# Performance work log

Measured on AMD Instinct MI355X. Metric: run time of the kernel, lower is better.

Reference implementation:

```python
import math
import jax, jax.numpy as jnp
import numpy as np
from jax import lax

SAMPLE_RATE = 16000
BLOCK_SIZE = 64
B = 524288


def setup_inputs() -> dict:
    key = jax.random.key(0)
    k1, k2, k3 = jax.random.split(key, 3)
    fm_params = jax.random.uniform(k1, (B, 1, 6), dtype=jnp.float32)
    # realistic fundamentals in [50, 400) Hz; module clamps to >=1 anyway
    f0_hz = 50.0 + 350.0 * jax.random.uniform(k2, (B, 1), dtype=jnp.float32)
    phase_state = jax.random.uniform(k3, (B, 4), dtype=jnp.float32)
    return {"fm_params": fm_params, "f0_hz": f0_hz, "phase_state": phase_state}


def reference(fm_params, f0_hz, phase_state):
    # T == 1 (module requirement), so squeeze the frame dim everywhere.
    dtype = fm_params.dtype
    two_pi = 2.0 * math.pi

    f0 = jnp.clip(f0_hz[:, 0], 1.0, None)            # [B]
    p = fm_params[:, 0, :]                            # [B, 6]
    # parameter mappings (op1 mod depth p[:,0] is unused, as in the original)
    r1 = 0.25 + p[:, 1] * 15.75
    fb1 = p[:, 2] * 0.95
    d2 = p[:, 3] * 10.0
    r2 = 0.25 + p[:, 4] * 15.75
    fb2 = p[:, 5] * 0.95

    inc1 = two_pi * f0 * r1 / SAMPLE_RATE             # [B]
    inc2 = two_pi * f0 * r2 / SAMPLE_RATE

    start1 = phase_state[:, 0]                        # frame start phases
    start2 = phase_state[:, 1]
    last1_0 = phase_state[:, 2]                       # feedback buffers
    last2_0 = phase_state[:, 3]

    offsets = jnp.arange(BLOCK_SIZE, dtype=dtype)     # [S]
    # per-sample phases, scanned over the sample axis: [S, B]
    phase1 = start1[None, :] + offsets[:, None] * inc1[None, :]
    phase2 = start2[None, :] + offsets[:, None] * inc2[None, :]

    def step(carry, ph):
        l1, l2 = carry
        ph1, ph2 = ph
        o1 = jnp.sin(ph1 + fb1 * l1)                  # op1 with self-feedback
        o2 = jnp.sin(ph2 + d2 * o1 + fb2 * l2)        # op2 carrier, FM'd by op1
        return (o1, o2), o2

    (l1f, l2f), samples = lax.scan(step, (last1_0, last2_0), (phase1, phase2))
    audio = samples.T                                 # [B, S]

    rms = jnp.sqrt(jnp.mean(audio * audio, axis=-1, keepdims=True) + 1e-5)
    audio = audio / rms

    phase_end = jnp.stack(
        [
            (start1 + BLOCK_SIZE * inc1) % two_pi,
            (start2 + BLOCK_SIZE * inc2) % two_pi,
            l1f,
            l2f,
        ],
        axis=-1,
    )                                                 # [B, 4]
    return audio, phase_end
```

## Files before the change

### kernel.cpp

```cpp
#include <hip/hip_runtime.h>

#define NBLOCK 64

__device__ __forceinline__ float fast_sinf(float x) {
    float kf = rintf(x * 0.63661977236758134f);
    int   q  = (int)kf;
    float r = fmaf(kf, -1.5707963705062866f, x);
    r = fmaf(kf, 4.3711390001862171e-8f, r);
    float z = r * r;
    float s = fmaf(z, fmaf(z, -1.9515295891e-4f, 8.3321608736e-3f), -1.6666654611e-1f);
    float sinr = fmaf(z * r, s, r);
    float c = fmaf(z, fmaf(z, 2.4433157118e-5f, -1.3887316255e-3f), 4.1666645683e-2f);
    float cosr = fmaf(z, fmaf(z, c, -0.5f), 1.0f);
    float res = (q & 1) ? cosr : sinr;
    return (q & 2) ? -res : res;
}

__device__ __forceinline__ float mod_two_pi(float x) {
    const float Y = 6.2831853071795864769f;
    float kf = floorf(__fdiv_rn(x, Y));
    float m = fmaf(-kf, Y, x);
    if (m < 0.0f)  { kf -= 1.0f; m = fmaf(-kf, Y, x); }
    if (m >= Y)    { kf += 1.0f; m = fmaf(-kf, Y, x); }
    return m;
}

__global__ __launch_bounds__(256)
void fm_synth_kernel(const float* __restrict__ fm_params,
                     const float* __restrict__ f0_hz,
                     const float* __restrict__ phase_state,
                     float* __restrict__ out, int nv)
{
    __shared__ float lds[256 * 17];

    int tid = threadIdx.x;
    int b   = blockIdx.x * 256 + tid;
    int bc  = min(b, nv - 1);
    bool live = (b < nv);

    const float2* fm2 = (const float2*)fm_params;
    float2 p01 = fm2[bc * 3 + 0];
    float2 p23 = fm2[bc * 3 + 1];
    float2 p45 = fm2[bc * 3 + 2];
    float  f0  = fmaxf(f0_hz[bc], 1.0f);
    float4 st  = ((const float4*)phase_state)[bc];

    const float TWO_PI = 6.2831853071795864769f;
    float r1  = __fadd_rn(0.25f, __fmul_rn(p01.y, 15.75f));
    float fb1 = __fmul_rn(p23.x, 0.95f);
    float d2  = __fmul_rn(p23.y, 10.0f);
    float r2  = __fadd_rn(0.25f, __fmul_rn(p45.x, 15.75f));
    float fb2 = __fmul_rn(p45.y, 0.95f);
    float inc1 = __fdiv_rn(__fmul_rn(__fmul_rn(TWO_PI, f0), r1), 16000.0f);
    float inc2 = __fdiv_rn(__fmul_rn(__fmul_rn(TWO_PI, f0), r2), 16000.0f);

    float start1 = st.x, start2 = st.y;
    float l1 = st.z, l2 = st.w;

    float smp[NBLOCK];
#pragma unroll
    for (int t = 0; t < NBLOCK; ++t) {
        float tf  = (float)t;
        float ph1 = tf * inc1 + start1;
        float ph2 = tf * inc2 + start2;
        float o1 = fast_sinf(ph1 + fb1 * l1);
        float o2 = fast_sinf(ph2 + d2 * o1 + fb2 * l2);
        l1 = o1;
        l2 = o2;
        smp[t] = o2;
    }

    float ss = 0.0f;
#pragma unroll
    for (int t = 0; t < NBLOCK; ++t) ss = fmaf(smp[t], smp[t], ss);
    float inv = 1.0f / sqrtf(ss * 0.015625f + 1e-5f);
#pragma unroll
    for (int t = 0; t < NBLOCK; ++t) smp[t] *= inv;

    float4* out4 = (float4*)out;
    int blockBase = blockIdx.x * 256;
    int u  = tid & 3;
    int v0 = tid >> 2;
#pragma unroll
    for (int c = 0; c < 4; ++c) {
        __syncthreads();
        float* slot = &lds[tid * 17];
#pragma unroll
        for (int i = 0; i < 16; ++i) slot[i] = smp[c * 16 + i];
        __syncthreads();
#pragma unroll
        for (int k = 0; k < 4; ++k) {
            int v = v0 + 64 * k;
            const float* src = &lds[v * 17 + u * 4];
            float4 val;
            val.x = src[0]; val.y = src[1]; val.z = src[2]; val.w = src[3];
            if (blockBase + v < nv)
                out4[(size_t)(blockBase + v) * 16 + 4 * c + u] = val;
        }
    }

    float x1 = __fadd_rn(start1, __fmul_rn(64.0f, inc1));
    float x2 = __fadd_rn(start2, __fmul_rn(64.0f, inc2));
    float4 pe;
    pe.x = mod_two_pi(x1);
    pe.y = mod_two_pi(x2);
    pe.z = l1;
    pe.w = l2;
    if (live)
        ((float4*)(out + (size_t)nv * NBLOCK))[b] = pe;
}

extern "C" void kernel_launch(void* const* d_in, const int* in_sizes, int n_in,
                              void* d_out, int out_size, void* d_ws, size_t ws_size,
                              hipStream_t stream) {
    const float* fm_params   = (const float*)d_in[0];
    const float* f0_hz       = (const float*)d_in[1];
    const float* phase_state = (const float*)d_in[2];
    float* out = (float*)d_out;
    int nv = in_sizes[1];
    int grid = (nv + 255) / 256;
    fm_synth_kernel<<<grid, 256, 0, stream>>>(fm_params, f0_hz, phase_state, out, nv);
}
```

Before: 171.4 us.

## Stream samples straight to swizzled LDS and fuse RMS scaling into transposed store

Each sample is written into a 64x256 swizzled shared-memory tile as soon as it is computed, and the sum of squares is accumulated on the fly. This replaces the 64-float register array and the four-pass transpose with its repeated barriers. The normalization is applied at store time, with each row's inverse RMS fetched by a wavefront shuffle. LDS use rises to 64 KB per block, which limits how many blocks can be resident per CU, but register pressure drops and only one barrier remains.

```diff
diff --git a/kernel.cpp b/kernel.cpp
--- a/kernel.cpp
+++ b/kernel.cpp
@@ -31,7 +31,7 @@
                      const float* __restrict__ phase_state,
                      float* __restrict__ out, int nv)
 {
-    __shared__ float lds[256 * 17];
+    __shared__ float lds[NBLOCK * 256];
 
     int tid = threadIdx.x;
     int b   = blockIdx.x * 256 + tid;
@@ -57,9 +57,11 @@
     float start1 = st.x, start2 = st.y;
     float l1 = st.z, l2 = st.w;
 
-    float smp[NBLOCK];
+    float ss = 0.0f;
+    int sw = tid;
 #pragma unroll
     for (int t = 0; t < NBLOCK; ++t) {
+        if ((t & 3) == 0) sw = (tid + t) & 255;
         float tf  = (float)t;
         float ph1 = tf * inc1 + start1;
         float ph2 = tf * inc2 + start2;
@@ -67,36 +69,33 @@
         float o2 = fast_sinf(ph2 + d2 * o1 + fb2 * l2);
         l1 = o1;
         l2 = o2;
-        smp[t] = o2;
+        lds[t * 256 + sw] = o2;
+        ss = fmaf(o2, o2, ss);
     }
+    float inv = 1.0f / sqrtf(ss * 0.015625f + 1e-5f);
 
-    float ss = 0.0f;
-#pragma unroll
-    for (int t = 0; t < NBLOCK; ++t) ss = fmaf(smp[t], smp[t], ss);
-    float inv = 1.0f / sqrtf(ss * 0.015625f + 1e-5f);
-#pragma unroll
-    for (int t = 0; t < NBLOCK; ++t) smp[t] *= inv;
+    __syncthreads();
 
+    int lane = tid & 63;
+    int w    = tid >> 6;
+    int q    = lane >> 4;
+    int t4   = lane & 15;
     float4* out4 = (float4*)out;
     int blockBase = blockIdx.x * 256;
-    int u  = tid & 3;
-    int v0 = tid >> 2;
 #pragma unroll
-    for (int c = 0; c < 4; ++c) {
-        __syncthreads();
-        float* slot = &lds[tid * 17];
-#pragma unroll
-        for (int i = 0; i < 16; ++i) slot[i] = smp[c * 16 + i];
-        __syncthreads();
-#pragma unroll
-        for (int k = 0; k < 4; ++k) {
-            int v = v0 + 64 * k;
-            const float* src = &lds[v * 17 + u * 4];
-            float4 val;
-            val.x = src[0]; val.y = src[1]; val.z = src[2]; val.w = src[3];
-            if (blockBase + v < nv)
-                out4[(size_t)(blockBase + v) * 16 + 4 * c + u] = val;
-        }
+    for (int k = 0; k < 16; ++k) {
+        int vv = 4 * k + q;
+        float invk = __shfl(inv, vv, 64);
+        int v = w * 64 + vv;
+        int sw2 = (v + 4 * t4) & 255;
+        const float* src = &lds[(4 * t4) * 256 + sw2];
+        float4 val;
+        val.x = src[0]     * invk;
+        val.y = src[256]   * invk;
+        val.z = src[512]   * invk;
+        val.w = src[768]   * invk;
+        if (blockBase + v < nv)
+            out4[(size_t)(blockBase + v) * 16 + t4] = val;
     }
 
     float x1 = __fadd_rn(start1, __fmul_rn(64.0f, inc1));
```

Result: slower. 177.1 us (+3.3%).
